# Kernel tuning notes

Hardware: AMD Instinct MI355X
Metric: run time of the kernel (lower is better)

The kernel has to match this reference:

```python
import jax, jax.numpy as jnp
import numpy as np

HIDDEN = 1024
HEADS = 16
HEAD_DIM = HIDDEN // HEADS


def setup_inputs() -> dict:
    key = jax.random.key(0)
    ks = jax.random.split(key, 9)
    B, S = 4, 2048
    s = 1.0 / np.sqrt(HIDDEN)
    return {
        "inputs": jax.random.normal(ks[0], (B, S, HIDDEN), dtype=jnp.float32),
        "Wq": jax.random.normal(ks[1], (HIDDEN, HIDDEN), dtype=jnp.float32) * s,
        "bq": jnp.zeros((HIDDEN,), dtype=jnp.float32),
        "Wk": jax.random.normal(ks[2], (HIDDEN, HIDDEN), dtype=jnp.float32) * s,
        "bk": jnp.zeros((HIDDEN,), dtype=jnp.float32),
        "Wv": jax.random.normal(ks[3], (HIDDEN, HIDDEN), dtype=jnp.float32) * s,
        "bv": jnp.zeros((HIDDEN,), dtype=jnp.float32),
        "Wp": jax.random.normal(ks[4], (HIDDEN, HIDDEN), dtype=jnp.float32) * s,
        "bp": jnp.zeros((HIDDEN,), dtype=jnp.float32),
        "heads_z": jnp.ones((1, HEADS, 1, 1), dtype=jnp.float32),
        "hidden_z": jnp.ones((HIDDEN,), dtype=jnp.float32),
    }


def _split_heads(x):
    # [B,S,HIDDEN] -> [B,H,S,Dh]
    B, S, _ = x.shape
    return x.reshape(B, S, HEADS, HEAD_DIM).transpose(0, 2, 1, 3)


def reference(inputs, Wq, bq, Wk, bk, Wv, bv, Wp, bp, heads_z, hidden_z):
    q = _split_heads(inputs @ Wq.T + bq)
    k = _split_heads(inputs @ Wk.T + bk)
    v = _split_heads(inputs @ Wv.T + bv)
    scores = jnp.einsum("bhqd,bhkd->bhqk", q, k) / jnp.sqrt(
        jnp.asarray(HEAD_DIM, dtype=q.dtype))
    probs = jax.nn.softmax(scores, axis=-1)
    ctx = jnp.einsum("bhqk,bhkd->bhqd", probs, v)  # [B,H,S,Dh]
    ctx = ctx * heads_z
    B, H, S, D = ctx.shape
    ctx = ctx.transpose(0, 2, 1, 3).reshape(B, S, H * D)
    out = ctx @ Wp.T + bp
    out = out * hidden_z
    return out
```

## Files before the change

### kernel.cpp

```cpp
#include <hip/hip_runtime.h>
#include <hip/hip_bf16.h>

#define HID 1024
#define NH 16
#define DH 64
#define SEQ 2048
#define NB 4
#define MTOT (NB*SEQ)
#define SM_SCALE 0.18033688f

typedef __attribute__((ext_vector_type(4))) float f32x4;
typedef __attribute__((ext_vector_type(16))) float f32x16;
typedef __attribute__((ext_vector_type(8))) __bf16 bf16x8;
typedef __attribute__((ext_vector_type(4))) __bf16 bf16x4;
typedef __attribute__((ext_vector_type(2))) __bf16 bf16x2;
typedef __attribute__((ext_vector_type(2))) int i32x2;

__device__ __forceinline__ f32x4 mfma16(bf16x8 a, bf16x8 b, f32x4 c) {
    return __builtin_amdgcn_mfma_f32_16x16x32_bf16(a, b, c, 0, 0, 0);
}
__device__ __forceinline__ f32x16 mfma32(bf16x8 a, bf16x8 b, f32x16 c) {
    return __builtin_amdgcn_mfma_f32_32x32x16_bf16(a, b, c, 0, 0, 0);
}

__device__ __forceinline__ void gload16(const void* g, void* l) {
    __builtin_amdgcn_global_load_lds(
        (const __attribute__((address_space(1))) unsigned int*)g,
        (__attribute__((address_space(3))) unsigned int*)l, 16, 0, 0);
}

__device__ __forceinline__ float fexp2(float x) {
#if __has_builtin(__builtin_amdgcn_exp2f)
    return __builtin_amdgcn_exp2f(x);
#else
    return exp2f(x);
#endif
}

__device__ __forceinline__ unsigned pkbf2(float lo, float hi) {
    union { bf16x2 v; unsigned u; } c;
    c.v = (bf16x2){ (__bf16)lo, (__bf16)hi };
    return c.u;
}

#define F3(a,b,c) fmaxf(fmaxf((a),(b)),(c))

__device__ __forceinline__ void swap32(unsigned &a, unsigned &b) {
#if __has_builtin(__builtin_amdgcn_permlane32_swap)
    i32x2 r = __builtin_amdgcn_permlane32_swap((int)a, (int)b, false, false);
    a = (unsigned)r.x; b = (unsigned)r.y;
#else
    const bool hi = (threadIdx.x & 32) != 0;
    unsigned ta = __shfl_xor(a, 32), tb = __shfl_xor(b, 32);
    unsigned na = hi ? tb : a;
    unsigned nb = hi ? b : ta;
    a = na; b = nb;
#endif
}

__device__ __forceinline__ float swapmaxf(float x) {
    unsigned a = __float_as_uint(x), b = a;
    swap32(a, b);
    return fmaxf(__uint_as_float(a), __uint_as_float(b));
}

__global__ __launch_bounds__(256)
void cvt5(const float* __restrict__ X,  const float* __restrict__ Wq,
          const float* __restrict__ Wk, const float* __restrict__ Wv,
          const float* __restrict__ Wp,
          __bf16* __restrict__ Xb,  __bf16* __restrict__ Wqb,
          __bf16* __restrict__ Wkb, __bf16* __restrict__ Wvb,
          __bf16* __restrict__ Wpb)
{
    const float* src; __bf16* dst; int n;
    switch (blockIdx.y) {
        case 0:  src = X;  dst = Xb;  n = MTOT * HID; break;
        case 1:  src = Wq; dst = Wqb; n = HID * HID;  break;
        case 2:  src = Wk; dst = Wkb; n = HID * HID;  break;
        case 3:  src = Wv; dst = Wvb; n = HID * HID;  break;
        default: src = Wp; dst = Wpb; n = HID * HID;  break;
    }
    const int stride = gridDim.x * 256 * 4;
    for (int i = (blockIdx.x * 256 + threadIdx.x) * 4; i < n; i += stride) {
        float4 v = *(const float4*)(src + i);
        bf16x4 o = { (__bf16)v.x, (__bf16)v.y, (__bf16)v.z, (__bf16)v.w };
        *(bf16x4*)(dst + i) = o;
    }
}

template<int PROJ>
__global__ __launch_bounds__(512, 1)
void gemm8(const __bf16* __restrict__ A,
           const __bf16* __restrict__ Wq, const __bf16* __restrict__ Wk,
           const __bf16* __restrict__ Wv,
           const float* __restrict__ bq, const float* __restrict__ bk,
           const float* __restrict__ bv, const float* __restrict__ hz,
           __bf16* __restrict__ Qo, __bf16* __restrict__ Ko,
           __bf16* __restrict__ Vo, float* __restrict__ Po)
{
    __shared__ __bf16 As[3][256 * 64];
    __shared__ __bf16 Bs[3][128 * 64];
    const int tid = threadIdx.x, lane = tid & 63, wid = tid >> 6;
    const int m0 = blockIdx.x * 256, n0 = blockIdx.y * 128;
    const int wr = wid >> 1, wc = wid & 1;
    const int mode = PROJ ? 3 : (int)blockIdx.z;

    const __bf16* W    = PROJ ? Wq : (mode == 0 ? Wq : mode == 1 ? Wk : Wv);
    const float*  bias = PROJ ? bq : (mode == 0 ? bq : mode == 1 ? bk : bv);

    const int cA0 = tid, cA1 = tid + 512, cA2 = tid + 1024, cA3 = tid + 1536;
    const int cB0 = tid, cB1 = tid + 512;
    const __bf16* aA0 = A + (size_t)(m0 + (cA0 >> 3)) * HID + ((cA0 & 7) ^ ((cA0 >> 3) & 7)) * 8;
    const __bf16* aA1 = A + (size_t)(m0 + (cA1 >> 3)) * HID + ((cA1 & 7) ^ ((cA1 >> 3) & 7)) * 8;
    const __bf16* aA2 = A + (size_t)(m0 + (cA2 >> 3)) * HID + ((cA2 & 7) ^ ((cA2 >> 3) & 7)) * 8;
    const __bf16* aA3 = A + (size_t)(m0 + (cA3 >> 3)) * HID + ((cA3 & 7) ^ ((cA3 >> 3) & 7)) * 8;
    const __bf16* bB0 = W + (size_t)(n0 + (cB0 >> 3)) * HID + ((cB0 & 7) ^ ((cB0 >> 3) & 7)) * 8;
    const __bf16* bB1 = W + (size_t)(n0 + (cB1 >> 3)) * HID + ((cB1 & 7) ^ ((cB1 >> 3) & 7)) * 8;

#define STAGE_A(sl, j) do { char* d_ = (char*)&As[sl][0]; int kk_ = (j) * 64; \
    gload16(aA0 + kk_, d_ + cA0 * 16); gload16(aA1 + kk_, d_ + cA1 * 16);     \
    gload16(aA2 + kk_, d_ + cA2 * 16); gload16(aA3 + kk_, d_ + cA3 * 16); } while (0)
#define STAGE_B(sl, j) do { char* d_ = (char*)&Bs[sl][0]; int kk_ = (j) * 64; \
    gload16(bB0 + kk_, d_ + cB0 * 16); gload16(bB1 + kk_, d_ + cB1 * 16); } while (0)

    f32x4 acc[4][4];
    #pragma unroll
    for (int i = 0; i < 4; i++)
        #pragma unroll
        for (int j = 0; j < 4; j++) acc[i][j] = (f32x4){0.f, 0.f, 0.f, 0.f};

    const int la = lane & 15, lk = lane >> 4;

    STAGE_A(0, 0); STAGE_B(0, 0);
    STAGE_A(1, 1); STAGE_B(1, 1);
    asm volatile("s_waitcnt vmcnt(6)" ::: "memory");
    __builtin_amdgcn_s_barrier();

    int slc = 0;
    for (int j = 0; j < 16; ++j) {
        const char* Ab = (const char*)&As[slc][0];
        const char* Bb = (const char*)&Bs[slc][0];
        const int js = j + 2;
        const int sls = slc == 0 ? 2 : slc - 1;

        bf16x8 af[4][2], bf0[2][2];
        #pragma unroll
        for (int mi = 0; mi < 4; mi++)
            #pragma unroll
            for (int ks = 0; ks < 2; ks++) {
                int row = wr * 64 + mi * 16 + la;
                af[mi][ks] = *(const bf16x8*)(Ab + row * 128 +
                    ((ks * 64 + lk * 16) ^ ((row & 7) << 4)));
            }
        #pragma unroll
        for (int ni = 0; ni < 2; ni++)
            #pragma unroll
            for (int ks = 0; ks < 2; ks++) {
                int row = wc * 64 + ni * 16 + la;
                bf0[ni][ks] = *(const bf16x8*)(Bb + row * 128 +
                    ((ks * 64 + lk * 16) ^ ((row & 7) << 4)));
            }
        if (js < 16) STAGE_A(sls, js);
        __builtin_amdgcn_s_barrier();
        asm volatile("s_waitcnt lgkmcnt(0)" ::: "memory");
        __builtin_amdgcn_sched_barrier(0);
        __builtin_amdgcn_s_setprio(1);
        #pragma unroll
        for (int mi = 0; mi < 4; mi++)
            #pragma unroll
            for (int ni = 0; ni < 2; ni++) {
                acc[mi][ni] = mfma16(af[mi][0], bf0[ni][0], acc[mi][ni]);
                acc[mi][ni] = mfma16(af[mi][1], bf0[ni][1], acc[mi][ni]);
            }
        __builtin_amdgcn_s_setprio(0);
        __builtin_amdgcn_s_barrier();

        bf16x8 bf1[2][2];
        #pragma unroll
        for (int ni = 0; ni < 2; ni++)
            #pragma unroll
            for (int ks = 0; ks < 2; ks++) {
                int row = wc * 64 + (ni + 2) * 16 + la;
                bf1[ni][ks] = *(const bf16x8*)(Bb + row * 128 +
                    ((ks * 64 + lk * 16) ^ ((row & 7) << 4)));
            }
        if (js < 16) STAGE_B(sls, js);
        __builtin_amdgcn_s_barrier();
        asm volatile("s_waitcnt lgkmcnt(0)" ::: "memory");
        __builtin_amdgcn_sched_barrier(0);
        __builtin_amdgcn_s_setprio(1);
        #pragma unroll
        for (int mi = 0; mi < 4; mi++)
            #pragma unroll
            for (int ni = 0; ni < 2; ni++) {
                acc[mi][ni + 2] = mfma16(af[mi][0], bf1[ni][0], acc[mi][ni + 2]);
                acc[mi][ni + 2] = mfma16(af[mi][1], bf1[ni][1], acc[mi][ni + 2]);
            }
        __builtin_amdgcn_s_setprio(0);

        if (j < 13)       { asm volatile("s_waitcnt vmcnt(6)" ::: "memory"); }
        else if (j == 14) { asm volatile("s_waitcnt vmcnt(0)" ::: "memory"); }
        __builtin_amdgcn_s_barrier();

        slc = slc == 2 ? 0 : slc + 1;
    }
#undef STAGE_A
#undef STAGE_B

    if (PROJ) {
        #pragma unroll
        for (int mi = 0; mi < 4; mi++)
            #pragma unroll
            for (int ni = 0; ni < 4; ni++)
                #pragma unroll
                for (int r = 0; r < 4; r++) {
                    int m = m0 + wr * 64 + mi * 16 + lk * 4 + r;
                    int n = n0 + wc * 64 + ni * 16 + la;
                    Po[(size_t)m * HID + n] = (acc[mi][ni][r] + bias[n]) * hz[n];
                }
    } else if (mode == 2) {
        #pragma unroll
        for (int mi = 0; mi < 4; mi++)
            #pragma unroll
            for (int ni = 0; ni < 4; ni++) {
                int m = m0 + wr * 64 + mi * 16 + lk * 4;
                int n = n0 + wc * 64 + ni * 16 + la;
                int b = m >> 11, s = m & (SEQ - 1);
                int h = n >> 6,  d = n & 63;
                bf16x4 o;
                #pragma unroll
                for (int r = 0; r < 4; r++) o[r] = (__bf16)(acc[mi][ni][r] + bias[n]);
                *(bf16x4*)(Vo + ((size_t)(b * NH + h) * DH + d) * SEQ + s) = o;
            }
    } else {
        const float qs = (mode == 0) ? SM_SCALE : 1.0f;
        __bf16* Og = (mode == 0) ? Qo : Ko;
        #pragma unroll
        for (int mi = 0; mi < 4; mi++)
            #pragma unroll
            for (int ni = 0; ni < 4; ni++)
                #pragma unroll
                for (int r = 0; r < 4; r++) {
                    int m = m0 + wr * 64 + mi * 16 + lk * 4 + r;
                    int n = n0 + wc * 64 + ni * 16 + la;
                    float v = (acc[mi][ni][r] + bias[n]) * qs;
                    int b = m >> 11, s = m & (SEQ - 1);
                    int h = n >> 6,  d = n & 63;
                    Og[((size_t)(b * NH + h) * SEQ + s) * DH + d] = (__bf16)v;
                }
    }
}

#define KVB 128

__global__ __launch_bounds__(512, 4)
void attn(const __bf16* __restrict__ Q, const __bf16* __restrict__ K,
          const __bf16* __restrict__ VT, const float* __restrict__ heads_z,
          __bf16* __restrict__ C)
{
    __shared__ __bf16 Ks[2][KVB * 64];
    __shared__ __bf16 Vs[2][64 * KVB];
    const int tid = threadIdx.x, lane = tid & 63, wid = tid >> 6;
    const int lh = lane >> 5;
    const int id = blockIdx.x;
    const int bh = (id & 7) | ((id >> 6) << 3);
    const int qb = (id >> 3) & 7;
    const int b = bh >> 4, hd = bh & 15;
    const __bf16* Qg = Q + (size_t)bh * SEQ * DH;
    const __bf16* Kg = K + (size_t)bh * SEQ * DH;
    const __bf16* Vg = VT + (size_t)bh * DH * SEQ;
    const int q = qb * 256 + wid * 32 + (lane & 31);
    const int r0 = lane & 31;
    const int kx = (r0 & 7) << 4;
    const int vx = (r0 & 15) << 4;

    bf16x8 ones8;
    #pragma unroll
    for (int j = 0; j < 8; j++) ones8[j] = (__bf16)1.0f;

    bf16x8 qf[4];
    #pragma unroll
    for (int s = 0; s < 4; s++)
        qf[s] = *(const bf16x8*)(Qg + (size_t)q * DH + s * 16 + lh * 8);

    f32x16 ctx0, ctx1;
    #pragma unroll
    for (int r = 0; r < 16; r++) { ctx0[r] = 0.f; ctx1[r] = 0.f; }
    float mrun = -1e30f, lrun = 0.f;

    const int kr0 = tid >> 3,          kss0 = (tid & 7) ^ (kr0 & 7);
    const int kr1 = (tid + 512) >> 3,  kss1 = (tid & 7) ^ (kr1 & 7);
    const int vr0 = tid >> 4,          vss0 = (tid & 15) ^ (vr0 & 15);
    const int vr1 = (tid + 512) >> 4,  vss1 = (tid & 15) ^ (vr1 & 15);

    gload16(Kg + (size_t)kr0 * DH + kss0 * 8, (char*)&Ks[0][0] + tid * 16);
    gload16(Kg + (size_t)kr1 * DH + kss1 * 8, (char*)&Ks[0][0] + (tid + 512) * 16);
    gload16(Vg + (size_t)vr0 * SEQ + 0 + vss0 * 8, (char*)&Vs[0][0] + tid * 16);
    gload16(Vg + (size_t)vr1 * SEQ + 0 + vss1 * 8, (char*)&Vs[0][0] + (tid + 512) * 16);
    __syncthreads();

    int cur = 0;
    for (int kv0 = 0; kv0 < SEQ; kv0 += KVB) {
        if (kv0 + KVB < SEQ) {
            int nx = kv0 + KVB;
            gload16(Kg + (size_t)(nx + kr0) * DH + kss0 * 8, (char*)&Ks[cur ^ 1][0] + tid * 16);
            gload16(Kg + (size_t)(nx + kr1) * DH + kss1 * 8, (char*)&Ks[cur ^ 1][0] + (tid + 512) * 16);
            gload16(Vg + (size_t)vr0 * SEQ + nx + vss0 * 8, (char*)&Vs[cur ^ 1][0] + tid * 16);
            gload16(Vg + (size_t)vr1 * SEQ + nx + vss1 * 8, (char*)&Vs[cur ^ 1][0] + (tid + 512) * 16);
        }

        #pragma unroll
        for (int hh = 0; hh < 2; hh++) {
            const char* Kb = (const char*)&Ks[cur][0] + hh * 64 * 128;
            const char* Vb = (const char*)&Vs[cur][0];

            f32x16 st0, st1;
            #pragma unroll
            for (int r = 0; r < 16; r++) { st0[r] = 0.f; st1[r] = 0.f; }
            __builtin_amdgcn_s_setprio(1);
            #pragma unroll
            for (int s = 0; s < 4; s++) {
                int co = (2 * s + lh) << 4;
                bf16x8 k0 = *(const bf16x8*)(Kb + r0 * 128 + (co ^ kx));
                bf16x8 k1 = *(const bf16x8*)(Kb + (r0 + 32) * 128 + (co ^ kx));
                st0 = mfma32(k0, qf[s], st0);
                st1 = mfma32(k1, qf[s], st1);
            }
            __builtin_amdgcn_s_setprio(0);

            float l1[11];
            l1[0] = F3(st0[0],  st0[1],  st0[2]);
            l1[1] = F3(st0[3],  st0[4],  st0[5]);
            l1[2] = F3(st0[6],  st0[7],  st0[8]);
            l1[3] = F3(st0[9],  st0[10], st0[11]);
            l1[4] = F3(st0[12], st0[13], st0[14]);
            l1[5] = F3(st0[15], st1[0],  st1[1]);
            l1[6] = F3(st1[2],  st1[3],  st1[4]);
            l1[7] = F3(st1[5],  st1[6],  st1[7]);
            l1[8] = F3(st1[8],  st1[9],  st1[10]);
            l1[9] = F3(st1[11], st1[12], st1[13]);
            l1[10] = fmaxf(st1[14], st1[15]);
            float l2a = F3(l1[0], l1[1], l1[2]);
            float l2b = F3(l1[3], l1[4], l1[5]);
            float l2c = F3(l1[6], l1[7], l1[8]);
            float l2d = fmaxf(l1[9], l1[10]);
            float pml = F3(F3(l2a, l2b, l2c), l2d, mrun);
            if (!__all(pml <= mrun + 8.f)) {
                float pm = swapmaxf(pml);
                float nm = fmaxf(mrun, pm);
                float al = fexp2(mrun - nm);
                lrun *= al; mrun = nm;
                #pragma unroll
                for (int r = 0; r < 16; r++) { ctx0[r] *= al; ctx1[r] *= al; }
            }
            const float mneg = -mrun;
            #pragma unroll
            for (int r = 0; r < 16; r++) {
                st0[r] = fexp2(st0[r] + mneg);
                st1[r] = fexp2(st1[r] + mneg);
            }

            unsigned X0 = pkbf2(st0[0],  st0[1]),  X1 = pkbf2(st0[2],  st0[3]);
            unsigned X2 = pkbf2(st0[4],  st0[5]),  X3 = pkbf2(st0[6],  st0[7]);
            unsigned X4 = pkbf2(st0[8],  st0[9]),  X5 = pkbf2(st0[10], st0[11]);
            unsigned X6 = pkbf2(st0[12], st0[13]), X7 = pkbf2(st0[14], st0[15]);
            unsigned Y0 = pkbf2(st1[0],  st1[1]),  Y1 = pkbf2(st1[2],  st1[3]);
            unsigned Y2 = pkbf2(st1[4],  st1[5]),  Y3 = pkbf2(st1[6],  st1[7]);
            unsigned Y4 = pkbf2(st1[8],  st1[9]),  Y5 = pkbf2(st1[10], st1[11]);
            unsigned Y6 = pkbf2(st1[12], st1[13]), Y7 = pkbf2(st1[14], st1[15]);
            swap32(X0, X2); swap32(X1, X3);
            swap32(X4, X6); swap32(X5, X7);
            swap32(Y0, Y2); swap32(Y1, Y3);
            swap32(Y4, Y6); swap32(Y5, Y7);
            union W4 { unsigned w[4]; bf16x8 v; };
            W4 pf[4];
            pf[0].w[0]=X0; pf[0].w[1]=X1; pf[0].w[2]=X2; pf[0].w[3]=X3;
            pf[1].w[0]=X4; pf[1].w[1]=X5; pf[1].w[2]=X6; pf[1].w[3]=X7;
            pf[2].w[0]=Y0; pf[2].w[1]=Y1; pf[2].w[2]=Y2; pf[2].w[3]=Y3;
            pf[3].w[0]=Y4; pf[3].w[1]=Y5; pf[3].w[2]=Y6; pf[3].w[3]=Y7;

            st0[0] = 0.f;
            #pragma unroll
            for (int s = 0; s < 4; s++) st0 = mfma32(ones8, pf[s].v, st0);

            __builtin_amdgcn_s_setprio(1);
            #pragma unroll
            for (int s = 0; s < 4; s++) {
                int co = (hh * 8 + 2 * s + lh) << 4;
                bf16x8 v0 = *(const bf16x8*)(Vb + r0 * 256 + (co ^ vx));
                bf16x8 v1 = *(const bf16x8*)(Vb + (r0 + 32) * 256 + (co ^ vx));
                ctx0 = mfma32(v0, pf[s].v, ctx0);
                ctx1 = mfma32(v1, pf[s].v, ctx1);
            }
            __builtin_amdgcn_s_setprio(0);

            lrun += st0[0];
        }

        __syncthreads();
        cur ^= 1;
    }

    const float hzv = heads_z[hd];
    const float rl = hzv / lrun;
    __bf16* Crow = C + (size_t)(b * SEQ + q) * HID + hd * DH;
    #pragma unroll
    for (int g = 0; g < 4; g++) {
        bf16x4 o0, o1;
        #pragma unroll
        for (int j = 0; j < 4; j++) {
            o0[j] = (__bf16)(ctx0[4 * g + j] * rl);
            o1[j] = (__bf16)(ctx1[4 * g + j] * rl);
        }
        int d0 = 8 * g + 4 * lh;
        *(bf16x4*)(Crow + d0) = o0;
        *(bf16x4*)(Crow + 32 + d0) = o1;
    }
}

extern "C" void kernel_launch(void* const* d_in, const int* in_sizes, int n_in,
                              void* d_out, int out_size, void* d_ws, size_t ws_size,
                              hipStream_t stream)
{
    const float* X    = (const float*)d_in[0];
    const float* Wq   = (const float*)d_in[1];
    const float* bq   = (const float*)d_in[2];
    const float* Wk   = (const float*)d_in[3];
    const float* bk   = (const float*)d_in[4];
    const float* Wv   = (const float*)d_in[5];
    const float* bv   = (const float*)d_in[6];
    const float* Wp   = (const float*)d_in[7];
    const float* bp   = (const float*)d_in[8];
    const float* hz   = (const float*)d_in[9];
    const float* hidz = (const float*)d_in[10];

    __bf16* ws  = (__bf16*)d_ws;
    __bf16* Xb  = ws;
    __bf16* Wqb = Xb  + (size_t)MTOT * HID;
    __bf16* Wkb = Wqb + (size_t)HID * HID;
    __bf16* Wvb = Wkb + (size_t)HID * HID;
    __bf16* Wpb = Wvb + (size_t)HID * HID;
    __bf16* Qb  = Wpb + (size_t)HID * HID;
    __bf16* Kb  = Qb  + (size_t)MTOT * HID;
    __bf16* VTb = Kb  + (size_t)MTOT * HID;
    __bf16* Cb  = VTb + (size_t)MTOT * HID;

    cvt5<<<dim3(2048, 5), 256, 0, stream>>>(X, Wq, Wk, Wv, Wp, Xb, Wqb, Wkb, Wvb, Wpb);

    gemm8<0><<<dim3(MTOT / 256, HID / 128, 3), 512, 0, stream>>>(
        Xb, Wqb, Wkb, Wvb, bq, bk, bv, nullptr, Qb, Kb, VTb, nullptr);

    attn<<<dim3(512), 512, 0, stream>>>(Qb, Kb, VTb, hz, Cb);

    gemm8<1><<<dim3(MTOT / 256, HID / 128), 512, 0, stream>>>(
        Cb, Wpb, nullptr, nullptr, bp, nullptr, nullptr, hidz,
        nullptr, nullptr, nullptr, (float*)d_out);
}
```

Measured before the change: 195.6 us.

## Split KV range across two wave groups per attention block and merge partials

```diff
diff --git a/kernel.cpp b/kernel.cpp
--- a/kernel.cpp
+++ b/kernel.cpp
@@ -251,28 +251,29 @@
     }
 }
 
-#define KVB 128
-
 __global__ __launch_bounds__(512, 4)
 void attn(const __bf16* __restrict__ Q, const __bf16* __restrict__ K,
           const __bf16* __restrict__ VT, const float* __restrict__ heads_z,
           __bf16* __restrict__ C)
 {
-    __shared__ __bf16 Ks[2][KVB * 64];
-    __shared__ __bf16 Vs[2][64 * KVB];
+    __shared__ __align__(16) char ldsbuf[34816];
     const int tid = threadIdx.x, lane = tid & 63, wid = tid >> 6;
     const int lh = lane >> 5;
+    const int wq = wid & 3, wg = wid >> 2;
     const int id = blockIdx.x;
-    const int bh = (id & 7) | ((id >> 6) << 3);
-    const int qb = (id >> 3) & 7;
+    const int bh = (id & 7) | ((id >> 7) << 3);
+    const int qb = (id >> 3) & 15;
     const int b = bh >> 4, hd = bh & 15;
     const __bf16* Qg = Q + (size_t)bh * SEQ * DH;
     const __bf16* Kg = K + (size_t)bh * SEQ * DH;
     const __bf16* Vg = VT + (size_t)bh * DH * SEQ;
-    const int q = qb * 256 + wid * 32 + (lane & 31);
+    const int q = qb * 128 + wq * 32 + (lane & 31);
     const int r0 = lane & 31;
     const int kx = (r0 & 7) << 4;
-    const int vx = (r0 & 15) << 4;
+    const int kvbase = wg * (SEQ / 2);
+
+    char* Kbase = ldsbuf + wg * 16384;
+    char* Vbase = Kbase + 8192;
 
     bf16x8 ones8;
     #pragma unroll
@@ -288,133 +289,150 @@
     for (int r = 0; r < 16; r++) { ctx0[r] = 0.f; ctx1[r] = 0.f; }
     float mrun = -1e30f, lrun = 0.f;
 
-    const int kr0 = tid >> 3,          kss0 = (tid & 7) ^ (kr0 & 7);
-    const int kr1 = (tid + 512) >> 3,  kss1 = (tid & 7) ^ (kr1 & 7);
-    const int vr0 = tid >> 4,          vss0 = (tid & 15) ^ (vr0 & 15);
-    const int vr1 = (tid + 512) >> 4,  vss1 = (tid & 15) ^ (vr1 & 15);
-
-    gload16(Kg + (size_t)kr0 * DH + kss0 * 8, (char*)&Ks[0][0] + tid * 16);
-    gload16(Kg + (size_t)kr1 * DH + kss1 * 8, (char*)&Ks[0][0] + (tid + 512) * 16);
-    gload16(Vg + (size_t)vr0 * SEQ + 0 + vss0 * 8, (char*)&Vs[0][0] + tid * 16);
-    gload16(Vg + (size_t)vr1 * SEQ + 0 + vss1 * 8, (char*)&Vs[0][0] + (tid + 512) * 16);
+    const int gt = tid & 255;
+    const int c0 = gt, c1 = gt + 256;
+    const int kr0 = c0 >> 3, kss0 = (c0 & 7) ^ (kr0 & 7);
+    const int kr1 = c1 >> 3, kss1 = (c1 & 7) ^ (kr1 & 7);
+
+#define STAGE(kv0_) do {                                                      \
+    gload16(Kg + (size_t)((kv0_) + kr0) * DH + kss0 * 8, Kbase + c0 * 16);    \
+    gload16(Kg + (size_t)((kv0_) + kr1) * DH + kss1 * 8, Kbase + c1 * 16);    \
+    gload16(Vg + (size_t)kr0 * SEQ + (kv0_) + kss0 * 8, Vbase + c0 * 16);     \
+    gload16(Vg + (size_t)kr1 * SEQ + (kv0_) + kss1 * 8, Vbase + c1 * 16);     \
+} while (0)
+
+    STAGE(kvbase);
+    asm volatile("s_waitcnt vmcnt(0)" ::: "memory");
     __syncthreads();
 
-    int cur = 0;
-    for (int kv0 = 0; kv0 < SEQ; kv0 += KVB) {
-        if (kv0 + KVB < SEQ) {
-            int nx = kv0 + KVB;
-            gload16(Kg + (size_t)(nx + kr0) * DH + kss0 * 8, (char*)&Ks[cur ^ 1][0] + tid * 16);
-            gload16(Kg + (size_t)(nx + kr1) * DH + kss1 * 8, (char*)&Ks[cur ^ 1][0] + (tid + 512) * 16);
-            gload16(Vg + (size_t)vr0 * SEQ + nx + vss0 * 8, (char*)&Vs[cur ^ 1][0] + tid * 16);
-            gload16(Vg + (size_t)vr1 * SEQ + nx + vss1 * 8, (char*)&Vs[cur ^ 1][0] + (tid + 512) * 16);
-        }
-
-        #pragma unroll
-        for (int hh = 0; hh < 2; hh++) {
-            const char* Kb = (const char*)&Ks[cur][0] + hh * 64 * 128;
-            const char* Vb = (const char*)&Vs[cur][0];
-
-            f32x16 st0, st1;
-            #pragma unroll
-            for (int r = 0; r < 16; r++) { st0[r] = 0.f; st1[r] = 0.f; }
-            __builtin_amdgcn_s_setprio(1);
-            #pragma unroll
-            for (int s = 0; s < 4; s++) {
-                int co = (2 * s + lh) << 4;
-                bf16x8 k0 = *(const bf16x8*)(Kb + r0 * 128 + (co ^ kx));
-                bf16x8 k1 = *(const bf16x8*)(Kb + (r0 + 32) * 128 + (co ^ kx));
-                st0 = mfma32(k0, qf[s], st0);
-                st1 = mfma32(k1, qf[s], st1);
-            }
-            __builtin_amdgcn_s_setprio(0);
-
-            float l1[11];
-            l1[0] = F3(st0[0],  st0[1],  st0[2]);
-            l1[1] = F3(st0[3],  st0[4],  st0[5]);
-            l1[2] = F3(st0[6],  st0[7],  st0[8]);
-            l1[3] = F3(st0[9],  st0[10], st0[11]);
-            l1[4] = F3(st0[12], st0[13], st0[14]);
-            l1[5] = F3(st0[15], st1[0],  st1[1]);
-            l1[6] = F3(st1[2],  st1[3],  st1[4]);
-            l1[7] = F3(st1[5],  st1[6],  st1[7]);
-            l1[8] = F3(st1[8],  st1[9],  st1[10]);
-            l1[9] = F3(st1[11], st1[12], st1[13]);
-            l1[10] = fmaxf(st1[14], st1[15]);
-            float l2a = F3(l1[0], l1[1], l1[2]);
-            float l2b = F3(l1[3], l1[4], l1[5]);
-            float l2c = F3(l1[6], l1[7], l1[8]);
-            float l2d = fmaxf(l1[9], l1[10]);
-            float pml = F3(F3(l2a, l2b, l2c), l2d, mrun);
-            if (!__all(pml <= mrun + 8.f)) {
-                float pm = swapmaxf(pml);
-                float nm = fmaxf(mrun, pm);
-                float al = fexp2(mrun - nm);
-                lrun *= al; mrun = nm;
-                #pragma unroll
-                for (int r = 0; r < 16; r++) { ctx0[r] *= al; ctx1[r] *= al; }
-            }
-            const float mneg = -mrun;
-            #pragma unroll
-            for (int r = 0; r < 16; r++) {
-                st0[r] = fexp2(st0[r] + mneg);
-                st1[r] = fexp2(st1[r] + mneg);
-            }
-
-            unsigned X0 = pkbf2(st0[0],  st0[1]),  X1 = pkbf2(st0[2],  st0[3]);
-            unsigned X2 = pkbf2(st0[4],  st0[5]),  X3 = pkbf2(st0[6],  st0[7]);
-            unsigned X4 = pkbf2(st0[8],  st0[9]),  X5 = pkbf2(st0[10], st0[11]);
-            unsigned X6 = pkbf2(st0[12], st0[13]), X7 = pkbf2(st0[14], st0[15]);
-            unsigned Y0 = pkbf2(st1[0],  st1[1]),  Y1 = pkbf2(st1[2],  st1[3]);
-            unsigned Y2 = pkbf2(st1[4],  st1[5]),  Y3 = pkbf2(st1[6],  st1[7]);
-            unsigned Y4 = pkbf2(st1[8],  st1[9]),  Y5 = pkbf2(st1[10], st1[11]);
-            unsigned Y6 = pkbf2(st1[12], st1[13]), Y7 = pkbf2(st1[14], st1[15]);
-            swap32(X0, X2); swap32(X1, X3);
-            swap32(X4, X6); swap32(X5, X7);
-            swap32(Y0, Y2); swap32(Y1, Y3);
-            swap32(Y4, Y6); swap32(Y5, Y7);
-            union W4 { unsigned w[4]; bf16x8 v; };
-            W4 pf[4];
-            pf[0].w[0]=X0; pf[0].w[1]=X1; pf[0].w[2]=X2; pf[0].w[3]=X3;
-            pf[1].w[0]=X4; pf[1].w[1]=X5; pf[1].w[2]=X6; pf[1].w[3]=X7;
-            pf[2].w[0]=Y0; pf[2].w[1]=Y1; pf[2].w[2]=Y2; pf[2].w[3]=Y3;
-            pf[3].w[0]=Y4; pf[3].w[1]=Y5; pf[3].w[2]=Y6; pf[3].w[3]=Y7;
-
-            st0[0] = 0.f;
-            #pragma unroll
-            for (int s = 0; s < 4; s++) st0 = mfma32(ones8, pf[s].v, st0);
-
-            __builtin_amdgcn_s_setprio(1);
-            #pragma unroll
-            for (int s = 0; s < 4; s++) {
-                int co = (hh * 8 + 2 * s + lh) << 4;
-                bf16x8 v0 = *(const bf16x8*)(Vb + r0 * 256 + (co ^ vx));
-                bf16x8 v1 = *(const bf16x8*)(Vb + (r0 + 32) * 256 + (co ^ vx));
-                ctx0 = mfma32(v0, pf[s].v, ctx0);
-                ctx1 = mfma32(v1, pf[s].v, ctx1);
-            }
-            __builtin_amdgcn_s_setprio(0);
-
-            lrun += st0[0];
-        }
+    for (int t = 0; t < 16; ++t) {
+        const char* Kb = Kbase;
+        const char* Vb = Vbase;
+
+        f32x16 st0, st1;
+        #pragma unroll
+        for (int r = 0; r < 16; r++) { st0[r] = 0.f; st1[r] = 0.f; }
+        __builtin_amdgcn_s_setprio(1);
+        #pragma unroll
+        for (int s = 0; s < 4; s++) {
+            int co = (2 * s + lh) << 4;
+            bf16x8 k0 = *(const bf16x8*)(Kb + r0 * 128 + (co ^ kx));
+            bf16x8 k1 = *(const bf16x8*)(Kb + (r0 + 32) * 128 + (co ^ kx));
+            st0 = mfma32(k0, qf[s], st0);
+            st1 = mfma32(k1, qf[s], st1);
+        }
+        __builtin_amdgcn_s_setprio(0);
+
+        float l1[11];
+        l1[0] = F3(st0[0],  st0[1],  st0[2]);
+        l1[1] = F3(st0[3],  st0[4],  st0[5]);
+        l1[2] = F3(st0[6],  st0[7],  st0[8]);
+        l1[3] = F3(st0[9],  st0[10], st0[11]);
+        l1[4] = F3(st0[12], st0[13], st0[14]);
+        l1[5] = F3(st0[15], st1[0],  st1[1]);
+        l1[6] = F3(st1[2],  st1[3],  st1[4]);
+        l1[7] = F3(st1[5],  st1[6],  st1[7]);
+        l1[8] = F3(st1[8],  st1[9],  st1[10]);
+        l1[9] = F3(st1[11], st1[12], st1[13]);
+        l1[10] = fmaxf(st1[14], st1[15]);
+        float l2a = F3(l1[0], l1[1], l1[2]);
+        float l2b = F3(l1[3], l1[4], l1[5]);
+        float l2c = F3(l1[6], l1[7], l1[8]);
+        float l2d = fmaxf(l1[9], l1[10]);
+        float pml = F3(F3(l2a, l2b, l2c), l2d, mrun);
+        if (!__all(pml <= mrun + 8.f)) {
+            float pm = swapmaxf(pml);
+            float nm = fmaxf(mrun, pm);
+            float al = fexp2(mrun - nm);
+            lrun *= al; mrun = nm;
+            #pragma unroll
+            for (int r = 0; r < 16; r++) { ctx0[r] *= al; ctx1[r] *= al; }
+        }
+        const float mneg = -mrun;
+        #pragma unroll
+        for (int r = 0; r < 16; r++) {
+            st0[r] = fexp2(st0[r] + mneg);
+            st1[r] = fexp2(st1[r] + mneg);
+        }
+
+        unsigned X0 = pkbf2(st0[0],  st0[1]),  X1 = pkbf2(st0[2],  st0[3]);
+        unsigned X2 = pkbf2(st0[4],  st0[5]),  X3 = pkbf2(st0[6],  st0[7]);
+        unsigned X4 = pkbf2(st0[8],  st0[9]),  X5 = pkbf2(st0[10], st0[11]);
+        unsigned X6 = pkbf2(st0[12], st0[13]), X7 = pkbf2(st0[14], st0[15]);
+        unsigned Y0 = pkbf2(st1[0],  st1[1]),  Y1 = pkbf2(st1[2],  st1[3]);
+        unsigned Y2 = pkbf2(st1[4],  st1[5]),  Y3 = pkbf2(st1[6],  st1[7]);
+        unsigned Y4 = pkbf2(st1[8],  st1[9]),  Y5 = pkbf2(st1[10], st1[11]);
+        unsigned Y6 = pkbf2(st1[12], st1[13]), Y7 = pkbf2(st1[14], st1[15]);
+        swap32(X0, X2); swap32(X1, X3);
+        swap32(X4, X6); swap32(X5, X7);
+        swap32(Y0, Y2); swap32(Y1, Y3);
+        swap32(Y4, Y6); swap32(Y5, Y7);
+        union W4 { unsigned w[4]; bf16x8 v; };
+        W4 pf[4];
+        pf[0].w[0]=X0; pf[0].w[1]=X1; pf[0].w[2]=X2; pf[0].w[3]=X3;
+        pf[1].w[0]=X4; pf[1].w[1]=X5; pf[1].w[2]=X6; pf[1].w[3]=X7;
+        pf[2].w[0]=Y0; pf[2].w[1]=Y1; pf[2].w[2]=Y2; pf[2].w[3]=Y3;
+        pf[3].w[0]=Y4; pf[3].w[1]=Y5; pf[3].w[2]=Y6; pf[3].w[3]=Y7;
+
+        st0[0] = 0.f;
+        #pragma unroll
+        for (int s = 0; s < 4; s++) st0 = mfma32(ones8, pf[s].v, st0);
+
+        __builtin_amdgcn_s_setprio(1);
+        #pragma unroll
+        for (int s = 0; s < 4; s++) {
+            int co = (2 * s + lh) << 4;
+            bf16x8 v0 = *(const bf16x8*)(Vb + r0 * 128 + (co ^ kx));
+            bf16x8 v1 = *(const bf16x8*)(Vb + (r0 + 32) * 128 + (co ^ kx));
+            ctx0 = mfma32(v0, pf[s].v, ctx0);
+            ctx1 = mfma32(v1, pf[s].v, ctx1);
+        }
+        __builtin_amdgcn_s_setprio(0);
+
+        lrun += st0[0];
 
         __syncthreads();
-        cur ^= 1;
-    }
-
-    const float hzv = heads_z[hd];
-    const float rl = hzv / lrun;
-    __bf16* Crow = C + (size_t)(b * SEQ + q) * HID + hd * DH;
-    #pragma unroll
-    for (int g = 0; g < 4; g++) {
-        bf16x4 o0, o1;
-        #pragma unroll
-        for (int j = 0; j < 4; j++) {
-            o0[j] = (__bf16)(ctx0[4 * g + j] * rl);
-            o1[j] = (__bf16)(ctx1[4 * g + j] * rl);
-        }
-        int d0 = 8 * g + 4 * lh;
-        *(bf16x4*)(Crow + d0) = o0;
-        *(bf16x4*)(Crow + 32 + d0) = o1;
+        if (t + 1 < 16) {
+            STAGE(kvbase + (t + 1) * 64);
+            asm volatile("s_waitcnt vmcnt(0)" ::: "memory");
+        }
+        __syncthreads();
+    }
+#undef STAGE
+
+    float* mf = (float*)ldsbuf;
+    float* ml = (float*)(ldsbuf + 32768);
+    if (wg == 1) {
+        #pragma unroll
+        for (int j = 0; j < 16; j++) mf[wq * 2048 + j * 64 + lane] = ctx0[j];
+        #pragma unroll
+        for (int j = 0; j < 16; j++) mf[wq * 2048 + (16 + j) * 64 + lane] = ctx1[j];
+        ml[(wq * 64 + lane) * 2]     = mrun;
+        ml[(wq * 64 + lane) * 2 + 1] = lrun;
+    }
+    __syncthreads();
+    if (wg == 0) {
+        float mp = ml[(wq * 64 + lane) * 2];
+        float lp = ml[(wq * 64 + lane) * 2 + 1];
+        float nm = fmaxf(mrun, mp);
+        float a0 = fexp2(mrun - nm), a1 = fexp2(mp - nm);
+        float lall = lrun * a0 + lp * a1;
+        const float hzv = heads_z[hd];
+        const float rl0 = hzv * a0 / lall, rl1 = hzv * a1 / lall;
+        __bf16* Crow = C + (size_t)(b * SEQ + q) * HID + hd * DH;
+        #pragma unroll
+        for (int g = 0; g < 4; g++) {
+            bf16x4 o0, o1;
+            #pragma unroll
+            for (int j2 = 0; j2 < 4; j2++) {
+                int j = 4 * g + j2;
+                o0[j2] = (__bf16)(ctx0[j] * rl0 + mf[wq * 2048 + j * 64 + lane] * rl1);
+                o1[j2] = (__bf16)(ctx1[j] * rl0 + mf[wq * 2048 + (16 + j) * 64 + lane] * rl1);
+            }
+            int d0 = 8 * g + 4 * lh;
+            *(bf16x4*)(Crow + d0) = o0;
+            *(bf16x4*)(Crow + 32 + d0) = o1;
+        }
     }
 }
 
@@ -450,7 +468,7 @@
     gemm8<0><<<dim3(MTOT / 256, HID / 128, 3), 512, 0, stream>>>(
         Xb, Wqb, Wkb, Wvb, bq, bk, bv, nullptr, Qb, Kb, VTb, nullptr);
 
-    attn<<<dim3(512), 512, 0, stream>>>(Qb, Kb, VTb, hz, Cb);
+    attn<<<dim3(1024), 512, 0, stream>>>(Qb, Kb, VTb, hz, Cb);
 
     gemm8<1><<<dim3(MTOT / 256, HID / 128), 512, 0, stream>>>(
         Cb, Wpb, nullptr, nullptr, bp, nullptr, nullptr, hidz,
```

Result: no change. 197.0 us (+0.7%).
